# Kernel tuning notes

Measured on AMD Instinct MI355X. Metric: run time of the kernel, lower is better.

The kernel has to match this reference:

```python
import jax, jax.numpy as jnp
import numpy as np

B, N, E, C_IN, C_OUT = 4, 50000, 800000, 128, 128


def setup_inputs() -> dict:
    key = jax.random.key(0)
    k1, k2, k3, k4, k5 = jax.random.split(key, 5)
    x = jax.random.normal(k1, (B, N, C_IN), dtype=jnp.float32)
    edge_row = jax.random.randint(k2, (E,), 0, N, dtype=jnp.int32)
    edge_col = jax.random.randint(k3, (E,), 0, N, dtype=jnp.int32)
    edge_vals = jax.random.uniform(k4, (E,), dtype=jnp.float32)
    W = jax.random.normal(k5, (C_IN, C_OUT), dtype=jnp.float32) * 0.1  # weight_stddev=0.1
    b = jnp.full((C_OUT,), 0.1, dtype=jnp.float32)  # bias_constant=0.1
    return {"x": x, "edge_row": edge_row, "edge_col": edge_col,
            "edge_vals": edge_vals, "W": W, "b": b}


def reference(x, edge_row, edge_col, edge_vals, W, b):
    # Sparse adjacency aggregation: agg[b, r, :] = sum_e vals[e] * x[b, col[e], :]
    n = x.shape[1]

    def spmm(xb):  # xb: [N, C_in]
        msgs = xb[edge_col] * edge_vals[:, None]          # [E, C_in]
        return jax.ops.segment_sum(msgs, edge_row, num_segments=n)  # [N, C_in]

    agg = jax.vmap(spmm)(x)                               # [B, N, C_in]
    out = jnp.einsum('bnc,co->bno', agg, W) + b           # dense GEMM + bias
    return jax.nn.relu(out)
```

## Files before the change

kernel.cpp:

```cpp
#include <hip/hip_runtime.h>

#define NROWS 50000
#define BATCH 4
#define CH    128
#define CAP   64

typedef float  f32x4  __attribute__((ext_vector_type(4)));
typedef __bf16 bf16x8 __attribute__((ext_vector_type(8)));
typedef short  s16x8  __attribute__((ext_vector_type(8)));

static __device__ __forceinline__ unsigned short f2bf(float f) {
    unsigned u = __builtin_bit_cast(unsigned, f);
    u += 0x7fffu + ((u >> 16) & 1u);
    return (unsigned short)(u >> 16);
}

__global__ void k_scatter(const int* __restrict__ row, const int* __restrict__ col,
                          const float* __restrict__ vals, int E,
                          int* __restrict__ cnt, unsigned long long* __restrict__ csr) {
    int e = blockIdx.x * blockDim.x + threadIdx.x;
    if (e < E) {
        int r = row[e];
        int p = atomicAdd(&cnt[r], 1);
        if (p < CAP) {
            unsigned long long pk =
                (unsigned long long)(unsigned)col[e] |
                ((unsigned long long)__builtin_bit_cast(unsigned, vals[e]) << 32);
            csr[r * CAP + p] = pk;
        }
    }
}

__global__ __launch_bounds__(256) void k_xw(const float* __restrict__ x,
                                            const float* __restrict__ W,
                                            unsigned short* __restrict__ y) {
    __shared__ unsigned short WtL[128 * 136];
    __shared__ unsigned short yt[4][16 * 136];
    const int tid = threadIdx.x;
    for (int idx = tid; idx < 128 * 128; idx += 256) {
        int k = idx >> 7, n = idx & 127;
        WtL[n * 136 + k] = f2bf(W[idx]);
    }
    __syncthreads();

    const int wave = tid >> 6;
    const int lane = tid & 63;
    const int m    = lane & 15;
    const int quad = lane >> 4;
    unsigned short* __restrict__ myt = yt[wave];

    const int NSTRIP = (BATCH * NROWS) / 64;
    for (int s = blockIdx.x; s < NSTRIP; s += gridDim.x) {
        const int row0 = s * 64 + wave * 16;

        s16x8 a_s[4];
        const float* xr = x + (size_t)(row0 + m) * CH;
        #pragma unroll
        for (int kk = 0; kk < 4; ++kk) {
            const float4* p = (const float4*)(xr + kk * 32 + quad * 8);
            float4 f0 = p[0], f1 = p[1];
            s16x8 sv;
            sv[0] = f2bf(f0.x); sv[1] = f2bf(f0.y); sv[2] = f2bf(f0.z); sv[3] = f2bf(f0.w);
            sv[4] = f2bf(f1.x); sv[5] = f2bf(f1.y); sv[6] = f2bf(f1.z); sv[7] = f2bf(f1.w);
            a_s[kk] = sv;
        }

        #pragma unroll
        for (int nt = 0; nt < 8; ++nt) {
            f32x4 acc = {0.f, 0.f, 0.f, 0.f};
            #pragma unroll
            for (int kk = 0; kk < 4; ++kk) {
                bf16x8 b = *(const bf16x8*)&WtL[(nt * 16 + m) * 136 + kk * 32 + quad * 8];
                acc = __builtin_amdgcn_mfma_f32_16x16x32_bf16(
                          __builtin_bit_cast(bf16x8, a_s[kk]), b, acc, 0, 0, 0);
            }
            #pragma unroll
            for (int reg = 0; reg < 4; ++reg)
                myt[(quad * 4 + reg) * 136 + nt * 16 + m] = f2bf(acc[reg]);
        }

        #pragma unroll
        for (int it = 0; it < 4; ++it) {
            const int lrow = it * 4 + (lane >> 4);
            const int seg  = lane & 15;
            uint4 v = *(const uint4*)&myt[lrow * 136 + seg * 8];
            const int i  = row0 + lrow;
            const int bb = i / NROWS;
            const int n  = i - bb * NROWS;
            *(uint4*)&y[((size_t)n * BATCH + bb) * CH + seg * 8] = v;
        }
    }
}

__global__ __launch_bounds__(256) void k_spmm(const uint4* __restrict__ y4,
                                              const int* __restrict__ cnt,
                                              const unsigned long long* __restrict__ csr,
                                              const float* __restrict__ bias,
                                              float* __restrict__ out) {
    __shared__ unsigned long long lcsr[4][CAP];
    __shared__ float lout[4][512];
    const int tid  = threadIdx.x;
    const int wave = tid >> 6;
    const int lane = tid & 63;
    const int b    = lane >> 4;
    const int m    = lane & 15;
    const int r    = blockIdx.x * 4 + wave;
    const int deg  = min(cnt[r], CAP);
    if (lane < deg) lcsr[wave][lane] = csr[(size_t)r * CAP + lane];
    __syncthreads();

    const uint4* __restrict__ Yl = y4 + lane;
    float alo[4] = {0.f, 0.f, 0.f, 0.f};
    float ahi[4] = {0.f, 0.f, 0.f, 0.f};

    int e = 0;
    for (; e + 8 <= deg; e += 8) {
        unsigned long long pk[8];
        #pragma unroll
        for (int j = 0; j < 8; ++j) pk[j] = lcsr[wave][e + j];
        uint4 u[8];
        #pragma unroll
        for (int j = 0; j < 8; ++j) u[j] = Yl[(size_t)(unsigned)pk[j] * 64];
        #pragma unroll
        for (int j = 0; j < 8; ++j) {
            float v = __builtin_bit_cast(float, (unsigned)(pk[j] >> 32));
            alo[0] += v * __builtin_bit_cast(float, u[j].x << 16);
            ahi[0] += v * __builtin_bit_cast(float, u[j].x & 0xffff0000u);
            alo[1] += v * __builtin_bit_cast(float, u[j].y << 16);
            ahi[1] += v * __builtin_bit_cast(float, u[j].y & 0xffff0000u);
            alo[2] += v * __builtin_bit_cast(float, u[j].z << 16);
            ahi[2] += v * __builtin_bit_cast(float, u[j].z & 0xffff0000u);
            alo[3] += v * __builtin_bit_cast(float, u[j].w << 16);
            ahi[3] += v * __builtin_bit_cast(float, u[j].w & 0xffff0000u);
        }
    }
    for (; e < deg; ++e) {
        unsigned long long pk = lcsr[wave][e];
        float v = __builtin_bit_cast(float, (unsigned)(pk >> 32));
        uint4 u = Yl[(size_t)(unsigned)pk * 64];
        alo[0] += v * __builtin_bit_cast(float, u.x << 16);
        ahi[0] += v * __builtin_bit_cast(float, u.x & 0xffff0000u);
        alo[1] += v * __builtin_bit_cast(float, u.y << 16);
        ahi[1] += v * __builtin_bit_cast(float, u.y & 0xffff0000u);
        alo[2] += v * __builtin_bit_cast(float, u.z << 16);
        ahi[2] += v * __builtin_bit_cast(float, u.z & 0xffff0000u);
        alo[3] += v * __builtin_bit_cast(float, u.w << 16);
        ahi[3] += v * __builtin_bit_cast(float, u.w & 0xffff0000u);
    }

    #pragma unroll
    for (int k = 0; k < 4; ++k) {
        float2 bv = ((const float2*)bias)[4 * m + k];
        float ox = fmaxf(alo[k] + bv.x, 0.f);
        float oy = fmaxf(ahi[k] + bv.y, 0.f);
        *(float2*)&lout[wave][b * 128 + 8 * m + 2 * k] = make_float2(ox, oy);
    }

    const int bb  = lane >> 4;
    const int ch0 = (lane & 15) * 8;
    float* __restrict__ orow = out + ((size_t)bb * NROWS + r) * CH + ch0;
    #pragma unroll
    for (int k = 0; k < 4; ++k) {
        unsigned long long pv = *(const unsigned long long*)&lout[wave][lane * 8 + 2 * k];
        __builtin_nontemporal_store(pv, (unsigned long long*)(orow + 2 * k));
    }
}

extern "C" void kernel_launch(void* const* d_in, const int* in_sizes, int n_in,
                              void* d_out, int out_size, void* d_ws, size_t ws_size,
                              hipStream_t stream) {
    const float* x        = (const float*)d_in[0];
    const int*   edge_row = (const int*)d_in[1];
    const int*   edge_col = (const int*)d_in[2];
    const float* edge_val = (const float*)d_in[3];
    const float* W        = (const float*)d_in[4];
    const float* bias     = (const float*)d_in[5];
    float*       out      = (float*)d_out;

    const int E = in_sizes[1];

    int*                cnt = (int*)d_ws;
    unsigned long long* csr = (unsigned long long*)(cnt + 50048);
    unsigned short*     y   = (unsigned short*)(csr + (size_t)NROWS * CAP);

    hipMemsetAsync(cnt, 0, 50048 * sizeof(int), stream);
    k_scatter<<<(E + 255) / 256, 256, 0, stream>>>(edge_row, edge_col, edge_val, E,
                                                   cnt, csr);
    k_xw<<<1250, 256, 0, stream>>>(x, W, y);
    k_spmm<<<NROWS / 4, 256, 0, stream>>>((const uint4*)y, cnt, csr, bias, out);
}
```

Before: 367.7 us.

## Enlarge XW blocks, pack spmm FMAs, and coalesce output stores across waves

The XW GEMM kernel now runs 512-thread blocks that each handle 128-row strips, so the W-to-LDS transpose is amortized over more rows. The spmm accumulators become float2 vectors so the compiler can emit packed FMA instructions. The output epilogue now sits behind one block-wide barrier, and each wave writes one batch slice across the block's 4 rows as contiguous 512-byte stores, with padded LDS rows to avoid bank conflicts. The early barrier after the CSR load is dropped, since each wave reads only its own CSR slice. The new late barrier makes waves wait for the slowest row in the block.

```diff
diff --git a/kernel.cpp b/kernel.cpp
--- a/kernel.cpp
+++ b/kernel.cpp
@@ -6,6 +6,7 @@
 #define CAP   64
 
 typedef float  f32x4  __attribute__((ext_vector_type(4)));
+typedef float  f32x2  __attribute__((ext_vector_type(2)));
 typedef __bf16 bf16x8 __attribute__((ext_vector_type(8)));
 typedef short  s16x8  __attribute__((ext_vector_type(8)));
 
@@ -31,13 +32,13 @@
     }
 }
 
-__global__ __launch_bounds__(256) void k_xw(const float* __restrict__ x,
-                                            const float* __restrict__ W,
-                                            unsigned short* __restrict__ y) {
+__global__ __launch_bounds__(512, 4) void k_xw(const float* __restrict__ x,
+                                               const float* __restrict__ W,
+                                               unsigned short* __restrict__ y) {
     __shared__ unsigned short WtL[128 * 136];
-    __shared__ unsigned short yt[4][16 * 136];
+    __shared__ unsigned short yt[8][16 * 136];
     const int tid = threadIdx.x;
-    for (int idx = tid; idx < 128 * 128; idx += 256) {
+    for (int idx = tid; idx < 128 * 128; idx += 512) {
         int k = idx >> 7, n = idx & 127;
         WtL[n * 136 + k] = f2bf(W[idx]);
     }
@@ -49,9 +50,10 @@
     const int quad = lane >> 4;
     unsigned short* __restrict__ myt = yt[wave];
 
-    const int NSTRIP = (BATCH * NROWS) / 64;
+    const int NSTRIP = (BATCH * NROWS + 127) / 128;
     for (int s = blockIdx.x; s < NSTRIP; s += gridDim.x) {
-        const int row0 = s * 64 + wave * 16;
+        const int row0 = s * 128 + wave * 16;
+        if (row0 >= BATCH * NROWS) continue;
 
         s16x8 a_s[4];
         const float* xr = x + (size_t)(row0 + m) * CH;
@@ -98,7 +100,7 @@
                                               const float* __restrict__ bias,
                                               float* __restrict__ out) {
     __shared__ unsigned long long lcsr[4][CAP];
-    __shared__ float lout[4][512];
+    __shared__ float lout[4][4 * 132];
     const int tid  = threadIdx.x;
     const int wave = tid >> 6;
     const int lane = tid & 63;
@@ -107,11 +109,11 @@
     const int r    = blockIdx.x * 4 + wave;
     const int deg  = min(cnt[r], CAP);
     if (lane < deg) lcsr[wave][lane] = csr[(size_t)r * CAP + lane];
-    __syncthreads();
 
     const uint4* __restrict__ Yl = y4 + lane;
-    float alo[4] = {0.f, 0.f, 0.f, 0.f};
-    float ahi[4] = {0.f, 0.f, 0.f, 0.f};
+    f32x2 acc[4];
+    #pragma unroll
+    for (int k = 0; k < 4; ++k) acc[k] = (f32x2){0.f, 0.f};
 
     int e = 0;
     for (; e + 8 <= deg; e += 8) {
@@ -124,45 +126,45 @@
         #pragma unroll
         for (int j = 0; j < 8; ++j) {
             float v = __builtin_bit_cast(float, (unsigned)(pk[j] >> 32));
-            alo[0] += v * __builtin_bit_cast(float, u[j].x << 16);
-            ahi[0] += v * __builtin_bit_cast(float, u[j].x & 0xffff0000u);
-            alo[1] += v * __builtin_bit_cast(float, u[j].y << 16);
-            ahi[1] += v * __builtin_bit_cast(float, u[j].y & 0xffff0000u);
-            alo[2] += v * __builtin_bit_cast(float, u[j].z << 16);
-            ahi[2] += v * __builtin_bit_cast(float, u[j].z & 0xffff0000u);
-            alo[3] += v * __builtin_bit_cast(float, u[j].w << 16);
-            ahi[3] += v * __builtin_bit_cast(float, u[j].w & 0xffff0000u);
+            unsigned uu[4] = {u[j].x, u[j].y, u[j].z, u[j].w};
+            #pragma unroll
+            for (int k = 0; k < 4; ++k) {
+                f32x2 p;
+                p[0] = __builtin_bit_cast(float, uu[k] << 16);
+                p[1] = __builtin_bit_cast(float, uu[k] & 0xffff0000u);
+                acc[k] += v * p;
+            }
         }
     }
     for (; e < deg; ++e) {
         unsigned long long pk = lcsr[wave][e];
         float v = __builtin_bit_cast(float, (unsigned)(pk >> 32));
         uint4 u = Yl[(size_t)(unsigned)pk * 64];
-        alo[0] += v * __builtin_bit_cast(float, u.x << 16);
-        ahi[0] += v * __builtin_bit_cast(float, u.x & 0xffff0000u);
-        alo[1] += v * __builtin_bit_cast(float, u.y << 16);
-        ahi[1] += v * __builtin_bit_cast(float, u.y & 0xffff0000u);
-        alo[2] += v * __builtin_bit_cast(float, u.z << 16);
-        ahi[2] += v * __builtin_bit_cast(float, u.z & 0xffff0000u);
-        alo[3] += v * __builtin_bit_cast(float, u.w << 16);
-        ahi[3] += v * __builtin_bit_cast(float, u.w & 0xffff0000u);
+        unsigned uu[4] = {u.x, u.y, u.z, u.w};
+        #pragma unroll
+        for (int k = 0; k < 4; ++k) {
+            f32x2 p;
+            p[0] = __builtin_bit_cast(float, uu[k] << 16);
+            p[1] = __builtin_bit_cast(float, uu[k] & 0xffff0000u);
+            acc[k] += v * p;
+        }
     }
 
     #pragma unroll
     for (int k = 0; k < 4; ++k) {
         float2 bv = ((const float2*)bias)[4 * m + k];
-        float ox = fmaxf(alo[k] + bv.x, 0.f);
-        float oy = fmaxf(ahi[k] + bv.y, 0.f);
-        *(float2*)&lout[wave][b * 128 + 8 * m + 2 * k] = make_float2(ox, oy);
+        float ox = fmaxf(acc[k][0] + bv.x, 0.f);
+        float oy = fmaxf(acc[k][1] + bv.y, 0.f);
+        *(float2*)&lout[wave][b * 132 + 8 * m + 2 * k] = make_float2(ox, oy);
     }
+    __syncthreads();
 
-    const int bb  = lane >> 4;
-    const int ch0 = (lane & 15) * 8;
-    float* __restrict__ orow = out + ((size_t)bb * NROWS + r) * CH + ch0;
     #pragma unroll
-    for (int k = 0; k < 4; ++k) {
-        unsigned long long pv = *(const unsigned long long*)&lout[wave][lane * 8 + 2 * k];
-        __builtin_nontemporal_store(pv, (unsigned long long*)(orow + 2 * k));
+    for (int t = 0; t < 4; ++t) {
+        unsigned long long pv = *(const unsigned long long*)&lout[t][wave * 132 + 2 * lane];
+        unsigned long long* dst =
+            (unsigned long long*)(out + ((size_t)wave * NROWS + blockIdx.x * 4 + t) * CH) + lane;
+        __builtin_nontemporal_store(pv, dst);
     }
 }
 
@@ -186,6 +188,6 @@
     hipMemsetAsync(cnt, 0, 50048 * sizeof(int), stream);
     k_scatter<<<(E + 255) / 256, 256, 0, stream>>>(edge_row, edge_col, edge_val, E,
                                                    cnt, csr);
-    k_xw<<<1250, 256, 0, stream>>>(x, W, y);
+    k_xw<<<1563, 512, 0, stream>>>(x, W, y);
     k_spmm<<<NROWS / 4, 256, 0, stream>>>((const uint4*)y, cnt, csr, bias, out);
 }
```

Result: faster. 360.4 us (-2.0%).
